# Kernel tuning notes

Measured on AMD Instinct MI355X. Metric: run time of the kernel, lower is better.

The kernel has to match this reference:

```python
import jax, jax.numpy as jnp
import numpy as np
import math

B, C, H, W = 32, 384, 64, 64      # batch, backbone dim, feature-map HxW
E, NH = 256, 16                   # embed_dim, num_heads (grapsules per image)
HD = E // NH                      # head dim
RFF_HALF, HID = 32, 128           # RFF rows (out=64), GNN hidden


def setup_inputs() -> dict:
    key = jax.random.key(0)
    ks = jax.random.split(key, 10)
    rn = lambda k, s: (0.02 * jax.random.normal(k, s)).astype(jnp.float32)
    x = jax.random.normal(ks[0], (B, C, H, W), jnp.float32)
    qw = rn(ks[1], (E, C)); qb = jnp.zeros((E,), jnp.float32)
    kw = rn(ks[2], (E, C)); kb = jnp.zeros((E,), jnp.float32)
    vw = rn(ks[3], (E, C)); vb = jnp.zeros((E,), jnp.float32)
    # RFF B ~ N(0,1) * sigma * 2*pi, sigma=1.0
    B_rff = (jax.random.normal(ks[4], (RFF_HALF, 2)) * (2.0 * math.pi)).astype(jnp.float32)
    msg_w = rn(ks[5], (HID, E)); msg_b = jnp.zeros((HID,), jnp.float32)
    emb_w = rn(ks[6], (HID, 2 * RFF_HALF))
    lin1_w = rn(ks[7], (4 * HID, HID)); lin1_b = jnp.zeros((4 * HID,), jnp.float32)
    lin2_w = rn(ks[8], (E, 4 * HID)); lin2_b = jnp.zeros((E,), jnp.float32)
    layer_scale = jnp.full((1, E), 1e-6, jnp.float32)
    # fully-connected directed graph (no self loops) among the NH grapsules of each image
    pairs = np.array([(i, j) for i in range(NH) for j in range(NH) if i != j], dtype=np.int32)
    off = (np.arange(B, dtype=np.int32) * NH)[:, None]
    edge_src = jnp.asarray((pairs[:, 0][None, :] + off).reshape(-1))
    edge_dst = jnp.asarray((pairs[:, 1][None, :] + off).reshape(-1))
    return dict(x=x, qw=qw, qb=qb, kw=kw, kb=kb, vw=vw, vb=vb, B_rff=B_rff,
                msg_w=msg_w, msg_b=msg_b, emb_w=emb_w, lin1_w=lin1_w, lin1_b=lin1_b,
                lin2_w=lin2_w, lin2_b=lin2_b, layer_scale=layer_scale,
                edge_src=edge_src, edge_dst=edge_dst)


def _forward(x, qw, qb, kw, kb, vw, vb, B_rff, msg_w, msg_b, emb_w,
             lin1_w, lin1_b, lin2_w, lin2_b, layer_scale, edge_src, edge_dst):
    Bsz, Cc, Hh, Ww = x.shape
    N = Hh * Ww
    # --- ImageToGraphTransformer (attention pooling to grapsule nodes) ---
    xf = x.reshape(Bsz, Cc, N).transpose(0, 2, 1)            # [B,N,C]
    xm = xf.mean(axis=1)                                     # [B,C]
    q = (xm @ qw.T + qb).reshape(Bsz, NH, HD)                # [B,h,d]
    k = (xf @ kw.T + kb).reshape(Bsz, N, NH, HD)             # [B,N,h,d]
    v = xf @ vw.T + vb                                       # [B,N,E]
    logits = jnp.einsum('bhc,bnhc->bnh', q, k) / math.sqrt(HD)
    attn = jax.nn.softmax(logits, axis=1)                    # softmax over pixels
    xx, yy = jnp.meshgrid(jnp.arange(Hh, dtype=x.dtype), jnp.arange(Ww, dtype=x.dtype), indexing='ij')
    pos_grid = jnp.stack((xx.reshape(-1), yy.reshape(-1)), axis=-1)  # [N,2]
    values = jnp.einsum('bnh,bnc->bhc', attn, v).reshape(Bsz * NH, E)
    pos = jnp.einsum('bnh,nx->bhx', attn, pos_grid).reshape(Bsz * NH, 2)
    # --- RFF embedding of relative positions (edge_attr) ---
    rel = pos[edge_src] - pos[edge_dst]                      # [Eg,2]
    proj = rel @ B_rff.T                                     # [Eg,32]
    edge_attr = math.sqrt(2.0) * jnp.concatenate((jnp.sin(proj), jnp.cos(proj)), axis=-1)
    # --- Conv (MessagePassing) with ConditionalLinear 'strong', mean aggr ---
    m = (values[edge_src] @ msg_w.T + msg_b) * (edge_attr @ emb_w.T)   # [Eg,HID]
    agg = jax.ops.segment_sum(m, edge_dst, num_segments=Bsz * NH) / (NH - 1)
    # --- ConvBlockNeXt MLP + layer scale + identity skip (in==out) ---
    h = jax.nn.silu(agg @ lin1_w.T + lin1_b)
    o = h @ lin2_w.T + lin2_b
    return layer_scale * o + values


def reference(x, qw, qb, kw, kb, vw, vb, B_rff, msg_w, msg_b, emb_w,
              lin1_w, lin1_b, lin2_w, lin2_b, layer_scale, edge_src, edge_dst):
    return _forward(x, qw, qb, kw, kb, vw, vb, B_rff, msg_w, msg_b, emb_w,
                    lin1_w, lin1_b, lin2_w, lin2_b, layer_scale, edge_src, edge_dst)
```

## Files before the change

### kernel.cpp

```cpp
#include <hip/hip_runtime.h>
#include <math.h>


#define Bsz 32
#define Cc  384
#define Nn  4096
#define Ee  256
#define NHh 16
#define HIDh 128

__device__ __forceinline__ float waveSum(float v){
#pragma unroll
  for(int o=32;o;o>>=1) v += __shfl_down(v,(unsigned)o,64);
  return v;
}
__device__ __forceinline__ float waveMaxAll(float v){
#pragma unroll
  for(int o=1;o<64;o<<=1) v = fmaxf(v, __shfl_xor(v,(unsigned)o,64));
  return v;
}
__device__ __forceinline__ float waveSumAll(float v){
#pragma unroll
  for(int o=1;o<64;o<<=1) v += __shfl_xor(v,(unsigned)o,64);
  return v;
}
__device__ __forceinline__ float blockSum(float v, float* sm){
  int lane = threadIdx.x & 63, w = threadIdx.x >> 6;
  int nw = blockDim.x >> 6;
  float r = waveSum(v);
  if(lane==0) sm[w] = r;
  __syncthreads();
  float s = 0.f;
  for(int i=0;i<nw;i++) s += sm[i];
  __syncthreads();
  return s;
}

__global__ __launch_bounds__(256) void k_mean(const float* __restrict__ x, float* __restrict__ xm){
  int bc = blockIdx.x, t = threadIdx.x;
  const float4* xr = (const float4*)(x + (size_t)bc*Nn);
  float s = 0.f;
#pragma unroll
  for(int i=0;i<4;i++){ float4 v = xr[t + 256*i]; s += (v.x+v.y) + (v.z+v.w); }
  __shared__ float sm[8];
  s = blockSum(s, sm);
  if(t==0) xm[bc] = s * (1.0f/4096.0f);
}

__global__ __launch_bounds__(384) void k_qk(const float* __restrict__ xm, const float* __restrict__ qw,
                                            const float* __restrict__ qb, const float* __restrict__ kw,
                                            float* __restrict__ qk_t){
  int b = blockIdx.x, t = threadIdx.x;
  __shared__ float xs[Cc];
  __shared__ float qs[Ee];
  if(t < 96) ((float4*)xs)[t] = ((const float4*)(xm + b*Cc))[t];
  __syncthreads();
  if(t < Ee){
    const float4* wr = (const float4*)(qw + (size_t)t*Cc);
    const float4* xv = (const float4*)xs;
    float a = qb[t];
#pragma unroll 4
    for(int c4=0;c4<96;c4++){ float4 w = wr[c4], xx = xv[c4]; a += w.x*xx.x + w.y*xx.y + w.z*xx.z + w.w*xx.w; }
    qs[t] = a;
  }
  __syncthreads();
  int c = t;
#pragma unroll
  for(int hq=0; hq<4; hq++){
    float r0, r1, r2, r3;
#pragma unroll
    for(int hh=0; hh<4; hh++){
      int h = hq*4 + hh;
      float a = 0.f;
#pragma unroll
      for(int d=0; d<16; d++) a += qs[h*16+d] * kw[(size_t)(h*16+d)*Cc + c];
      a *= 0.25f;
      if(hh==0) r0=a; else if(hh==1) r1=a; else if(hh==2) r2=a; else r3=a;
    }
    ((float4*)(qk_t + ((size_t)b*Cc + c)*16))[hq] = make_float4(r0,r1,r2,r3);
  }
}

__global__ __launch_bounds__(256) void k_logits(const float* __restrict__ x, const float* __restrict__ qk_t,
                                                float* __restrict__ lg, float* __restrict__ spart){
  __shared__ float qks[Cc*16];
  int b = blockIdx.y, ns = blockIdx.x, t = threadIdx.x;
  int n = ns*256 + t;
  {
    const float4* src = (const float4*)(qk_t + (size_t)b*Cc*16);
    float4* dst = (float4*)qks;
#pragma unroll
    for(int i=0;i<6;i++) dst[t + 256*i] = src[t + 256*i];
  }
  __syncthreads();
  float acc[16];
#pragma unroll
  for(int h=0;h<16;h++) acc[h] = 0.f;
  const float* xb = x + (size_t)b*Cc*Nn + n;
#pragma unroll 8
  for(int c=0;c<Cc;c++){
    float xv = xb[(size_t)c*Nn];
    const float4* qv = (const float4*)(qks + c*16);
    float4 q0 = qv[0], q1 = qv[1], q2 = qv[2], q3 = qv[3];
    acc[0]  += xv*q0.x; acc[1]  += xv*q0.y; acc[2]  += xv*q0.z; acc[3]  += xv*q0.w;
    acc[4]  += xv*q1.x; acc[5]  += xv*q1.y; acc[6]  += xv*q1.z; acc[7]  += xv*q1.w;
    acc[8]  += xv*q2.x; acc[9]  += xv*q2.y; acc[10] += xv*q2.z; acc[11] += xv*q2.w;
    acc[12] += xv*q3.x; acc[13] += xv*q3.y; acc[14] += xv*q3.z; acc[15] += xv*q3.w;
  }
#pragma unroll
  for(int h=0;h<16;h++) lg[((size_t)(b*16+h))*Nn + n] = acc[h];

  __syncthreads();
  float* sl = qks;
#pragma unroll
  for(int h=0;h<16;h++) sl[h*256 + t] = acc[h];
  __syncthreads();
  int w = t >> 6, lane = t & 63;
#pragma unroll
  for(int hh=0; hh<4; hh++){
    int h = w*4 + hh;
    float v0 = sl[h*256 + lane], v1 = sl[h*256 + 64 + lane];
    float v2 = sl[h*256 + 128 + lane], v3 = sl[h*256 + 192 + lane];
    float m = waveMaxAll(fmaxf(fmaxf(v0,v1), fmaxf(v2,v3)));
    float e0 = __expf(v0-m), e1 = __expf(v1-m), e2 = __expf(v2-m), e3 = __expf(v3-m);
    float row0 = (float)(ns*4);
    float col  = (float)lane;
    float s  = (e0+e1)+(e2+e3);
    float px = e0*row0 + e1*(row0+1.f) + e2*(row0+2.f) + e3*(row0+3.f);
    float py = s * col;
    float s_t  = waveSumAll(s);
    float px_t = waveSumAll(px);
    float py_t = waveSumAll(py);
    if(lane==0)
      *(float4*)(spart + ((size_t)(b*16+h)*16 + ns)*4) = make_float4(m, s_t, px_t, py_t);
  }
}

#define XROW 36
__global__ __launch_bounds__(256) void k_xa(const float* __restrict__ x, const float* __restrict__ lg,
                                            const float* __restrict__ spart, float* __restrict__ pos,
                                            float* __restrict__ part){
  __shared__ float xl[Cc*XROW];
  __shared__ float al[NHh*XROW];
  __shared__ float ss[32];
  int b = blockIdx.y, ns = blockIdx.x, t = threadIdx.x;
  int th = t & 3, tc = t >> 2;
  if(t < 64){
    int h = t >> 2, qq = t & 3;
    const float4* sp = (const float4*)spart + (size_t)(b*16+h)*16 + qq*4;
    float4 p0 = sp[0], p1 = sp[1], p2 = sp[2], p3 = sp[3];
    float m = fmaxf(fmaxf(p0.x,p1.x), fmaxf(p2.x,p3.x));
    m = fmaxf(m, __shfl_xor(m, 1u, 64));
    m = fmaxf(m, __shfl_xor(m, 2u, 64));
    float w0 = __expf(p0.x-m), w1 = __expf(p1.x-m), w2 = __expf(p2.x-m), w3 = __expf(p3.x-m);
    float s  = p0.y*w0 + p1.y*w1 + p2.y*w2 + p3.y*w3;
    float px = p0.z*w0 + p1.z*w1 + p2.z*w2 + p3.z*w3;
    float py = p0.w*w0 + p1.w*w1 + p2.w*w2 + p3.w*w3;
    s  += __shfl_xor(s, 1u, 64);  s  += __shfl_xor(s, 2u, 64);
    px += __shfl_xor(px,1u, 64);  px += __shfl_xor(px,2u, 64);
    py += __shfl_xor(py,1u, 64);  py += __shfl_xor(py,2u, 64);
    if(qq==0){
      float inv = 1.0f/s;
      ss[h*2] = m; ss[h*2+1] = inv;
      if(ns==0){ pos[(b*16+h)*2] = px*inv; pos[(b*16+h)*2+1] = py*inv; }
    }
  }
  __syncthreads();
  int ah = t >> 3, aj = t & 7;
  float mA = 0.f, iA = 0.f;
  if(t < 128){ mA = ss[ah*2]; iA = ss[ah*2+1]; }
  float acc[4][6];
#pragma unroll
  for(int k=0;k<4;k++)
#pragma unroll
    for(int m=0;m<6;m++) acc[k][m] = 0.f;

  float4 xr[12];
  float4 ar = make_float4(0,0,0,0);

  auto LOAD = [&](int ch){
    int n0 = ns*256 + ch*32;
    if(t < 128)
      ar = *(const float4*)(lg + ((size_t)(b*16+ah))*Nn + n0 + aj*4);
#pragma unroll
    for(int i=0;i<12;i++){
      int f = t + 256*i;
      int c = f >> 3, j4 = f & 7;
      xr[i] = *(const float4*)(x + ((size_t)(b*Cc+c))*Nn + n0 + j4*4);
    }
  };

  LOAD(0);
  for(int ch=0; ch<8; ch++){
    if(t < 128){
      float4 e;
      e.x = __expf(ar.x - mA)*iA;
      e.y = __expf(ar.y - mA)*iA;
      e.z = __expf(ar.z - mA)*iA;
      e.w = __expf(ar.w - mA)*iA;
      *(float4*)(al + ah*XROW + aj*4) = e;
    }
#pragma unroll
    for(int i=0;i<12;i++){
      int f = t + 256*i;
      int c = f >> 3, j4 = f & 7;
      *(float4*)(xl + c*XROW + j4*4) = xr[i];
    }
    __syncthreads();
    if(ch < 7) LOAD(ch+1);
#pragma unroll
    for(int j4=0;j4<8;j4++){
      float4 a4[4], x4[6];
#pragma unroll
      for(int k=0;k<4;k++) a4[k] = *(const float4*)(al + (th+4*k)*XROW + j4*4);
#pragma unroll
      for(int m=0;m<6;m++) x4[m] = *(const float4*)(xl + (tc+64*m)*XROW + j4*4);
#pragma unroll
      for(int k=0;k<4;k++)
#pragma unroll
        for(int m=0;m<6;m++)
          acc[k][m] += a4[k].x*x4[m].x + a4[k].y*x4[m].y + a4[k].z*x4[m].z + a4[k].w*x4[m].w;
    }
    __syncthreads();
  }
#pragma unroll
  for(int k=0;k<4;k++)
#pragma unroll
    for(int m=0;m<6;m++)
      part[(size_t)ns*(Bsz*NHh*Cc) + (size_t)(b*16 + th + 4*k)*Cc + (tc + 64*m)] = acc[k][m];
}

__global__ __launch_bounds__(256) void k_values(const float* __restrict__ part, const float* __restrict__ vw,
                                                const float* __restrict__ vb, const float* __restrict__ msg_w,
                                                const float* __restrict__ msg_b,
                                                float* __restrict__ values, float* __restrict__ msgv){
  int node = blockIdx.x, t = threadIdx.x;
  __shared__ float xa[Cc];
  __shared__ float vs[Ee];
  if(t < 96){
    float4 s = make_float4(0,0,0,0);
#pragma unroll
    for(int p=0;p<16;p++){
      float4 v = *(const float4*)(part + (size_t)p*(Bsz*NHh*Cc) + (size_t)node*Cc + t*4);
      s.x += v.x; s.y += v.y; s.z += v.z; s.w += v.w;
    }
    *(float4*)(xa + t*4) = s;
  }
  __syncthreads();
  {
    const float4* wr = (const float4*)(vw + (size_t)t*Cc);
    const float4* xv = (const float4*)xa;
    float a = vb[t];
#pragma unroll 4
    for(int c4=0;c4<96;c4++){ float4 w = wr[c4], xx = xv[c4]; a += w.x*xx.x + w.y*xx.y + w.z*xx.z + w.w*xx.w; }
    values[(size_t)node*Ee + t] = a;
    vs[t] = a;
  }
  __syncthreads();
  if(t < HIDh){
    const float4* mr = (const float4*)(msg_w + (size_t)t*Ee);
    const float4* vv = (const float4*)vs;
    float a = msg_b[t];
#pragma unroll 4
    for(int e4=0;e4<64;e4++){ float4 w = mr[e4], xx = vv[e4]; a += w.x*xx.x + w.y*xx.y + w.z*xx.z + w.w*xx.w; }
    msgv[(size_t)node*HIDh + t] = a;
  }
}

__global__ __launch_bounds__(128) void k_agg(const float* __restrict__ pos, const float* __restrict__ msgv,
                                             const float* __restrict__ brff, const float* __restrict__ emb_w,
                                             float* __restrict__ agg){
  int node = blockIdx.x, t = threadIdx.x;
  int b = node >> 4, jj = node & 15;
  __shared__ float ps[32];
  __shared__ float bf[64];
  __shared__ float mv[16*HIDh];
  __shared__ float ea[64];
  if(t < 32) ps[t] = pos[b*32 + t];
  if(t < 64) bf[t] = brff[t];
#pragma unroll
  for(int i=0;i<4;i++){ int f = t + 128*i; ((float4*)mv)[f] = ((const float4*)(msgv + (size_t)b*16*HIDh))[f]; }
  float4 er[16];
#pragma unroll
  for(int i=0;i<16;i++) er[i] = ((const float4*)(emb_w + (size_t)t*64))[i];
  __syncthreads();
  float pxj = ps[jj*2], pyj = ps[jj*2+1];
  float acc = 0.f;
  for(int i=0;i<16;i++){
    if(i == jj) continue;
    float rx = ps[i*2]   - pxj;
    float ry = ps[i*2+1] - pyj;
    __syncthreads();
    if(t < 32){
      float pr = rx*bf[t*2] + ry*bf[t*2+1];
      ea[t]    = 1.41421356f * __sinf(pr);
      ea[t+32] = 1.41421356f * __cosf(pr);
    }
    __syncthreads();
    float psi = 0.f;
    const float4* eav = (const float4*)ea;
#pragma unroll
    for(int k=0;k<16;k++){ float4 e4 = eav[k]; psi += e4.x*er[k].x + e4.y*er[k].y + e4.z*er[k].z + e4.w*er[k].w; }
    acc += mv[i*HIDh + t] * psi;
  }
  agg[(size_t)node*HIDh + t] = acc * (1.0f/15.0f);
}

__global__ __launch_bounds__(256) void k_mlp(const float* __restrict__ agg, const float* __restrict__ l1w,
                                             const float* __restrict__ l1b, const float* __restrict__ l2w,
                                             const float* __restrict__ l2b, const float* __restrict__ ls,
                                             const float* __restrict__ values, float* __restrict__ out){
  int node = blockIdx.x, t = threadIdx.x;
  __shared__ float ag[HIDh];
  __shared__ float h1[512];
  if(t < 32) ((float4*)ag)[t] = ((const float4*)(agg + (size_t)node*HIDh))[t];
  __syncthreads();
#pragma unroll
  for(int r=0;r<2;r++){
    int u = t + r*256;
    const float4* wr = (const float4*)(l1w + (size_t)u*HIDh);
    const float4* av = (const float4*)ag;
    float a = l1b[u];
#pragma unroll 4
    for(int k=0;k<32;k++){ float4 w = wr[k], xx = av[k]; a += w.x*xx.x + w.y*xx.y + w.z*xx.z + w.w*xx.w; }
    h1[u] = a / (1.0f + __expf(-a));
  }
  __syncthreads();
  {
    const float4* wr = (const float4*)(l2w + (size_t)t*512);
    const float4* hv = (const float4*)h1;
    float o = l2b[t];
#pragma unroll 4
    for(int k=0;k<128;k++){ float4 w = wr[k], xx = hv[k]; o += w.x*xx.x + w.y*xx.y + w.z*xx.z + w.w*xx.w; }
    size_t oi = (size_t)node*Ee + t;
    out[oi] = ls[t]*o + values[oi];
  }
}

extern "C" void kernel_launch(void* const* d_in, const int* in_sizes, int n_in,
                              void* d_out, int out_size, void* d_ws, size_t ws_size,
                              hipStream_t stream) {
  const float* x    = (const float*)d_in[0];
  const float* qw   = (const float*)d_in[1];
  const float* qb   = (const float*)d_in[2];
  const float* kw   = (const float*)d_in[3];
  const float* vw   = (const float*)d_in[5];
  const float* vb   = (const float*)d_in[6];
  const float* brff = (const float*)d_in[7];
  const float* msgw = (const float*)d_in[8];
  const float* msgb = (const float*)d_in[9];
  const float* embw = (const float*)d_in[10];
  const float* l1w  = (const float*)d_in[11];
  const float* l1b  = (const float*)d_in[12];
  const float* l2w  = (const float*)d_in[13];
  const float* l2b  = (const float*)d_in[14];
  const float* lsc  = (const float*)d_in[15];

  float* W      = (float*)d_ws;
  float* xm     = W;
  float* qkt    = xm  + 12288;
  float* lg     = qkt + 196608;
  float* pos    = lg  + 2097152;
  float* spart  = pos + 1024;
  float* part   = spart + 32768;
  float* values = part + 3145728;
  float* msgv   = values + 131072;
  float* agg    = msgv + 65536;
  float* out    = (float*)d_out;

  k_mean  <<<Bsz*Cc, 256, 0, stream>>>(x, xm);
  k_qk    <<<Bsz, 384, 0, stream>>>(xm, qw, qb, kw, qkt);
  k_logits<<<dim3(16, Bsz), 256, 0, stream>>>(x, qkt, lg, spart);
  k_xa    <<<dim3(16, Bsz), 256, 0, stream>>>(x, lg, spart, pos, part);
  k_values<<<Bsz*NHh, 256, 0, stream>>>(part, vw, vb, msgw, msgb, values, msgv);
  k_agg   <<<Bsz*NHh, 128, 0, stream>>>(pos, msgv, brff, embw, agg);
  k_mlp   <<<Bsz*NHh, 256, 0, stream>>>(agg, l1w, l1b, l2w, l2b, lsc, values, out);
}
```

Measured before the change: 564.9 us.

## Split k_xa over channel halves and read qk directly from global in k_logits

k_xa now splits the 384 channels into two halves across blocks, so the grid doubles to 1024 blocks. Each block uses half the shared memory and accumulators, which is meant to raise occupancy and parallelism on a grid that was previously only 512 blocks. Partial sums go into 32 slots, and k_values is changed to reduce the two halves from separate slot ranges. Separately, k_logits stops staging qk in LDS and reads it straight from global/cache, dropping a sync and 24KB of shared memory. The cost is that the logits and softmax coefficients are recomputed per half-block, and the x reads in k_logits now compete with uniform global loads of qk.

New measurement: 579.5 us. +2.6%, slower.

```diff
diff --git a/kernel.cpp b/kernel.cpp
--- a/kernel.cpp
+++ b/kernel.cpp
@@ -83,25 +83,18 @@
 
 __global__ __launch_bounds__(256) void k_logits(const float* __restrict__ x, const float* __restrict__ qk_t,
                                                 float* __restrict__ lg, float* __restrict__ spart){
-  __shared__ float qks[Cc*16];
+  __shared__ float sl[16*256];
   int b = blockIdx.y, ns = blockIdx.x, t = threadIdx.x;
   int n = ns*256 + t;
-  {
-    const float4* src = (const float4*)(qk_t + (size_t)b*Cc*16);
-    float4* dst = (float4*)qks;
-#pragma unroll
-    for(int i=0;i<6;i++) dst[t + 256*i] = src[t + 256*i];
-  }
-  __syncthreads();
   float acc[16];
 #pragma unroll
   for(int h=0;h<16;h++) acc[h] = 0.f;
   const float* xb = x + (size_t)b*Cc*Nn + n;
+  const float4* qk = (const float4*)(qk_t + (size_t)b*Cc*16);
 #pragma unroll 8
   for(int c=0;c<Cc;c++){
     float xv = xb[(size_t)c*Nn];
-    const float4* qv = (const float4*)(qks + c*16);
-    float4 q0 = qv[0], q1 = qv[1], q2 = qv[2], q3 = qv[3];
+    float4 q0 = qk[c*4+0], q1 = qk[c*4+1], q2 = qk[c*4+2], q3 = qk[c*4+3];
     acc[0]  += xv*q0.x; acc[1]  += xv*q0.y; acc[2]  += xv*q0.z; acc[3]  += xv*q0.w;
     acc[4]  += xv*q1.x; acc[5]  += xv*q1.y; acc[6]  += xv*q1.z; acc[7]  += xv*q1.w;
     acc[8]  += xv*q2.x; acc[9]  += xv*q2.y; acc[10] += xv*q2.z; acc[11] += xv*q2.w;
@@ -110,8 +103,6 @@
 #pragma unroll
   for(int h=0;h<16;h++) lg[((size_t)(b*16+h))*Nn + n] = acc[h];
 
-  __syncthreads();
-  float* sl = qks;
 #pragma unroll
   for(int h=0;h<16;h++) sl[h*256 + t] = acc[h];
   __syncthreads();
@@ -137,13 +128,16 @@
 }
 
 #define XROW 36
+#define CSPL 192
+#define SLOTSZ (512*CSPL)
 __global__ __launch_bounds__(256) void k_xa(const float* __restrict__ x, const float* __restrict__ lg,
                                             const float* __restrict__ spart, float* __restrict__ pos,
                                             float* __restrict__ part){
-  __shared__ float xl[Cc*XROW];
+  __shared__ float xl[CSPL*XROW];
   __shared__ float al[NHh*XROW];
   __shared__ float ss[32];
-  int b = blockIdx.y, ns = blockIdx.x, t = threadIdx.x;
+  int b = blockIdx.y, t = threadIdx.x;
+  int ns = blockIdx.x & 15, cs = blockIdx.x >> 4;
   int th = t & 3, tc = t >> 2;
   if(t < 64){
     int h = t >> 2, qq = t & 3;
@@ -162,31 +156,32 @@
     if(qq==0){
       float inv = 1.0f/s;
       ss[h*2] = m; ss[h*2+1] = inv;
-      if(ns==0){ pos[(b*16+h)*2] = px*inv; pos[(b*16+h)*2+1] = py*inv; }
+      if(blockIdx.x==0){ pos[(b*16+h)*2] = px*inv; pos[(b*16+h)*2+1] = py*inv; }
     }
   }
   __syncthreads();
   int ah = t >> 3, aj = t & 7;
   float mA = 0.f, iA = 0.f;
   if(t < 128){ mA = ss[ah*2]; iA = ss[ah*2+1]; }
-  float acc[4][6];
+  float acc[4][3];
 #pragma unroll
   for(int k=0;k<4;k++)
 #pragma unroll
-    for(int m=0;m<6;m++) acc[k][m] = 0.f;
-
-  float4 xr[12];
+    for(int m=0;m<3;m++) acc[k][m] = 0.f;
+
+  float4 xr[6];
   float4 ar = make_float4(0,0,0,0);
+  const float* xbase = x + ((size_t)b*Cc + (size_t)cs*CSPL)*Nn;
 
   auto LOAD = [&](int ch){
     int n0 = ns*256 + ch*32;
     if(t < 128)
       ar = *(const float4*)(lg + ((size_t)(b*16+ah))*Nn + n0 + aj*4);
 #pragma unroll
-    for(int i=0;i<12;i++){
+    for(int i=0;i<6;i++){
       int f = t + 256*i;
       int c = f >> 3, j4 = f & 7;
-      xr[i] = *(const float4*)(x + ((size_t)(b*Cc+c))*Nn + n0 + j4*4);
+      xr[i] = *(const float4*)(xbase + (size_t)c*Nn + n0 + j4*4);
     }
   };
 
@@ -201,7 +196,7 @@
       *(float4*)(al + ah*XROW + aj*4) = e;
     }
 #pragma unroll
-    for(int i=0;i<12;i++){
+    for(int i=0;i<6;i++){
       int f = t + 256*i;
       int c = f >> 3, j4 = f & 7;
       *(float4*)(xl + c*XROW + j4*4) = xr[i];
@@ -210,24 +205,25 @@
     if(ch < 7) LOAD(ch+1);
 #pragma unroll
     for(int j4=0;j4<8;j4++){
-      float4 a4[4], x4[6];
+      float4 a4[4], x4[3];
 #pragma unroll
       for(int k=0;k<4;k++) a4[k] = *(const float4*)(al + (th+4*k)*XROW + j4*4);
 #pragma unroll
-      for(int m=0;m<6;m++) x4[m] = *(const float4*)(xl + (tc+64*m)*XROW + j4*4);
+      for(int m=0;m<3;m++) x4[m] = *(const float4*)(xl + (tc+64*m)*XROW + j4*4);
 #pragma unroll
       for(int k=0;k<4;k++)
 #pragma unroll
-        for(int m=0;m<6;m++)
+        for(int m=0;m<3;m++)
           acc[k][m] += a4[k].x*x4[m].x + a4[k].y*x4[m].y + a4[k].z*x4[m].z + a4[k].w*x4[m].w;
     }
     __syncthreads();
   }
+  size_t slot = (size_t)(cs*16 + ns)*SLOTSZ;
 #pragma unroll
   for(int k=0;k<4;k++)
 #pragma unroll
-    for(int m=0;m<6;m++)
-      part[(size_t)ns*(Bsz*NHh*Cc) + (size_t)(b*16 + th + 4*k)*Cc + (tc + 64*m)] = acc[k][m];
+    for(int m=0;m<3;m++)
+      part[slot + (size_t)(b*16 + th + 4*k)*CSPL + (tc + 64*m)] = acc[k][m];
 }
 
 __global__ __launch_bounds__(256) void k_values(const float* __restrict__ part, const float* __restrict__ vw,
@@ -238,10 +234,12 @@
   __shared__ float xa[Cc];
   __shared__ float vs[Ee];
   if(t < 96){
+    int half = (t >= 48);
+    const float* base = part + (size_t)(half*16)*SLOTSZ + (size_t)node*CSPL + (t*4 - half*CSPL);
     float4 s = make_float4(0,0,0,0);
 #pragma unroll
     for(int p=0;p<16;p++){
-      float4 v = *(const float4*)(part + (size_t)p*(Bsz*NHh*Cc) + (size_t)node*Cc + t*4);
+      float4 v = *(const float4*)(base + (size_t)p*SLOTSZ);
       s.x += v.x; s.y += v.y; s.z += v.z; s.w += v.w;
     }
     *(float4*)(xa + t*4) = s;
@@ -371,7 +369,7 @@
   k_mean  <<<Bsz*Cc, 256, 0, stream>>>(x, xm);
   k_qk    <<<Bsz, 384, 0, stream>>>(xm, qw, qb, kw, qkt);
   k_logits<<<dim3(16, Bsz), 256, 0, stream>>>(x, qkt, lg, spart);
-  k_xa    <<<dim3(16, Bsz), 256, 0, stream>>>(x, lg, spart, pos, part);
+  k_xa    <<<dim3(32, Bsz), 256, 0, stream>>>(x, lg, spart, pos, part);
   k_values<<<Bsz*NHh, 256, 0, stream>>>(part, vw, vb, msgw, msgb, values, msgv);
   k_agg   <<<Bsz*NHh, 128, 0, stream>>>(pos, msgv, brff, embw, agg);
   k_mlp   <<<Bsz*NHh, 256, 0, stream>>>(agg, l1w, l1b, l2w, l2b, lsc, values, out);
```

## Fuse logits and attention pooling with flash-style partial softmax rescaling

Applied to the files above, without the earlier changes.

Merges the logits kernel and the attention-weighted pooling kernel into one. Each block keeps its unnormalized exponentials in shared memory, writes unnormalized partial pooled sums, and the values kernel rescales the partials using the per-tile max and sum statistics. This removes the global logits buffer round trip and a second pass reading the logits. The aggregation and MLP kernels are also merged, and the qk table is now read directly from global memory instead of staged in LDS. The cost is higher LDS use per block, which can lower occupancy.

Result: slower. 585.8 us (+3.7%).

```diff
diff --git a/kernel.cpp b/kernel.cpp
--- a/kernel.cpp
+++ b/kernel.cpp
@@ -81,107 +81,70 @@
   }
 }
 
-__global__ __launch_bounds__(256) void k_logits(const float* __restrict__ x, const float* __restrict__ qk_t,
-                                                float* __restrict__ lg, float* __restrict__ spart){
-  __shared__ float qks[Cc*16];
+#define XROW 36
+#define ELS  260
+__global__ __launch_bounds__(256) void k_attn(const float* __restrict__ x, const float* __restrict__ qk_t,
+                                              float* __restrict__ spart, float* __restrict__ part){
+  __shared__ float el[16*ELS];
+  __shared__ float xl[Cc*XROW];
   int b = blockIdx.y, ns = blockIdx.x, t = threadIdx.x;
   int n = ns*256 + t;
+
+  float acc[16];
+#pragma unroll
+  for(int h=0;h<16;h++) acc[h] = 0.f;
   {
-    const float4* src = (const float4*)(qk_t + (size_t)b*Cc*16);
-    float4* dst = (float4*)qks;
-#pragma unroll
-    for(int i=0;i<6;i++) dst[t + 256*i] = src[t + 256*i];
-  }
-  __syncthreads();
-  float acc[16];
-#pragma unroll
-  for(int h=0;h<16;h++) acc[h] = 0.f;
-  const float* xb = x + (size_t)b*Cc*Nn + n;
-#pragma unroll 8
-  for(int c=0;c<Cc;c++){
-    float xv = xb[(size_t)c*Nn];
-    const float4* qv = (const float4*)(qks + c*16);
-    float4 q0 = qv[0], q1 = qv[1], q2 = qv[2], q3 = qv[3];
-    acc[0]  += xv*q0.x; acc[1]  += xv*q0.y; acc[2]  += xv*q0.z; acc[3]  += xv*q0.w;
-    acc[4]  += xv*q1.x; acc[5]  += xv*q1.y; acc[6]  += xv*q1.z; acc[7]  += xv*q1.w;
-    acc[8]  += xv*q2.x; acc[9]  += xv*q2.y; acc[10] += xv*q2.z; acc[11] += xv*q2.w;
-    acc[12] += xv*q3.x; acc[13] += xv*q3.y; acc[14] += xv*q3.z; acc[15] += xv*q3.w;
-  }
-#pragma unroll
-  for(int h=0;h<16;h++) lg[((size_t)(b*16+h))*Nn + n] = acc[h];
-
-  __syncthreads();
-  float* sl = qks;
-#pragma unroll
-  for(int h=0;h<16;h++) sl[h*256 + t] = acc[h];
-  __syncthreads();
-  int w = t >> 6, lane = t & 63;
-#pragma unroll
-  for(int hh=0; hh<4; hh++){
-    int h = w*4 + hh;
-    float v0 = sl[h*256 + lane], v1 = sl[h*256 + 64 + lane];
-    float v2 = sl[h*256 + 128 + lane], v3 = sl[h*256 + 192 + lane];
-    float m = waveMaxAll(fmaxf(fmaxf(v0,v1), fmaxf(v2,v3)));
-    float e0 = __expf(v0-m), e1 = __expf(v1-m), e2 = __expf(v2-m), e3 = __expf(v3-m);
-    float row0 = (float)(ns*4);
-    float col  = (float)lane;
-    float s  = (e0+e1)+(e2+e3);
-    float px = e0*row0 + e1*(row0+1.f) + e2*(row0+2.f) + e3*(row0+3.f);
-    float py = s * col;
-    float s_t  = waveSumAll(s);
-    float px_t = waveSumAll(px);
-    float py_t = waveSumAll(py);
-    if(lane==0)
-      *(float4*)(spart + ((size_t)(b*16+h)*16 + ns)*4) = make_float4(m, s_t, px_t, py_t);
-  }
-}
-
-#define XROW 36
-__global__ __launch_bounds__(256) void k_xa(const float* __restrict__ x, const float* __restrict__ lg,
-                                            const float* __restrict__ spart, float* __restrict__ pos,
-                                            float* __restrict__ part){
-  __shared__ float xl[Cc*XROW];
-  __shared__ float al[NHh*XROW];
-  __shared__ float ss[32];
-  int b = blockIdx.y, ns = blockIdx.x, t = threadIdx.x;
+    const float* xb = x + (size_t)b*Cc*Nn + n;
+    const float4* qk = (const float4*)(qk_t + (size_t)b*Cc*16);
+#pragma unroll 16
+    for(int c=0;c<Cc;c++){
+      float xv = xb[(size_t)c*Nn];
+      float4 q0 = qk[c*4+0], q1 = qk[c*4+1], q2 = qk[c*4+2], q3 = qk[c*4+3];
+      acc[0]  += xv*q0.x; acc[1]  += xv*q0.y; acc[2]  += xv*q0.z; acc[3]  += xv*q0.w;
+      acc[4]  += xv*q1.x; acc[5]  += xv*q1.y; acc[6]  += xv*q1.z; acc[7]  += xv*q1.w;
+      acc[8]  += xv*q2.x; acc[9]  += xv*q2.y; acc[10] += xv*q2.z; acc[11] += xv*q2.w;
+      acc[12] += xv*q3.x; acc[13] += xv*q3.y; acc[14] += xv*q3.z; acc[15] += xv*q3.w;
+    }
+  }
+
+#pragma unroll
+  for(int h=0;h<16;h++) el[h*ELS + t] = acc[h];
+  __syncthreads();
+  {
+    int w = t >> 6, lane = t & 63;
+#pragma unroll
+    for(int hh=0; hh<4; hh++){
+      int h = w*4 + hh;
+      float v0 = el[h*ELS + lane],       v1 = el[h*ELS + 64 + lane];
+      float v2 = el[h*ELS + 128 + lane], v3 = el[h*ELS + 192 + lane];
+      float m = waveMaxAll(fmaxf(fmaxf(v0,v1), fmaxf(v2,v3)));
+      float e0 = __expf(v0-m), e1 = __expf(v1-m), e2 = __expf(v2-m), e3 = __expf(v3-m);
+      el[h*ELS + lane]       = e0;  el[h*ELS + 64 + lane]  = e1;
+      el[h*ELS + 128 + lane] = e2;  el[h*ELS + 192 + lane] = e3;
+      float row0 = (float)(ns*4);
+      float col  = (float)lane;
+      float s  = (e0+e1)+(e2+e3);
+      float px = e0*row0 + e1*(row0+1.f) + e2*(row0+2.f) + e3*(row0+3.f);
+      float py = s * col;
+      float s_t  = waveSumAll(s);
+      float px_t = waveSumAll(px);
+      float py_t = waveSumAll(py);
+      if(lane==0)
+        *(float4*)(spart + ((size_t)(b*16+h)*16 + ns)*4) = make_float4(m, s_t, px_t, py_t);
+    }
+  }
+  __syncthreads();
+
   int th = t & 3, tc = t >> 2;
-  if(t < 64){
-    int h = t >> 2, qq = t & 3;
-    const float4* sp = (const float4*)spart + (size_t)(b*16+h)*16 + qq*4;
-    float4 p0 = sp[0], p1 = sp[1], p2 = sp[2], p3 = sp[3];
-    float m = fmaxf(fmaxf(p0.x,p1.x), fmaxf(p2.x,p3.x));
-    m = fmaxf(m, __shfl_xor(m, 1u, 64));
-    m = fmaxf(m, __shfl_xor(m, 2u, 64));
-    float w0 = __expf(p0.x-m), w1 = __expf(p1.x-m), w2 = __expf(p2.x-m), w3 = __expf(p3.x-m);
-    float s  = p0.y*w0 + p1.y*w1 + p2.y*w2 + p3.y*w3;
-    float px = p0.z*w0 + p1.z*w1 + p2.z*w2 + p3.z*w3;
-    float py = p0.w*w0 + p1.w*w1 + p2.w*w2 + p3.w*w3;
-    s  += __shfl_xor(s, 1u, 64);  s  += __shfl_xor(s, 2u, 64);
-    px += __shfl_xor(px,1u, 64);  px += __shfl_xor(px,2u, 64);
-    py += __shfl_xor(py,1u, 64);  py += __shfl_xor(py,2u, 64);
-    if(qq==0){
-      float inv = 1.0f/s;
-      ss[h*2] = m; ss[h*2+1] = inv;
-      if(ns==0){ pos[(b*16+h)*2] = px*inv; pos[(b*16+h)*2+1] = py*inv; }
-    }
-  }
-  __syncthreads();
-  int ah = t >> 3, aj = t & 7;
-  float mA = 0.f, iA = 0.f;
-  if(t < 128){ mA = ss[ah*2]; iA = ss[ah*2+1]; }
-  float acc[4][6];
+  float acc2[4][6];
 #pragma unroll
   for(int k=0;k<4;k++)
 #pragma unroll
-    for(int m=0;m<6;m++) acc[k][m] = 0.f;
+    for(int m=0;m<6;m++) acc2[k][m] = 0.f;
 
   float4 xr[12];
-  float4 ar = make_float4(0,0,0,0);
-
   auto LOAD = [&](int ch){
     int n0 = ns*256 + ch*32;
-    if(t < 128)
-      ar = *(const float4*)(lg + ((size_t)(b*16+ah))*Nn + n0 + aj*4);
 #pragma unroll
     for(int i=0;i<12;i++){
       int f = t + 256*i;
@@ -192,14 +155,6 @@
 
   LOAD(0);
   for(int ch=0; ch<8; ch++){
-    if(t < 128){
-      float4 e;
-      e.x = __expf(ar.x - mA)*iA;
-      e.y = __expf(ar.y - mA)*iA;
-      e.z = __expf(ar.z - mA)*iA;
-      e.w = __expf(ar.w - mA)*iA;
-      *(float4*)(al + ah*XROW + aj*4) = e;
-    }
 #pragma unroll
     for(int i=0;i<12;i++){
       int f = t + 256*i;
@@ -208,18 +163,19 @@
     }
     __syncthreads();
     if(ch < 7) LOAD(ch+1);
+    int n0l = ch*32;
 #pragma unroll
     for(int j4=0;j4<8;j4++){
       float4 a4[4], x4[6];
 #pragma unroll
-      for(int k=0;k<4;k++) a4[k] = *(const float4*)(al + (th+4*k)*XROW + j4*4);
+      for(int k=0;k<4;k++) a4[k] = *(const float4*)(el + (th+4*k)*ELS + n0l + j4*4);
 #pragma unroll
       for(int m=0;m<6;m++) x4[m] = *(const float4*)(xl + (tc+64*m)*XROW + j4*4);
 #pragma unroll
       for(int k=0;k<4;k++)
 #pragma unroll
         for(int m=0;m<6;m++)
-          acc[k][m] += a4[k].x*x4[m].x + a4[k].y*x4[m].y + a4[k].z*x4[m].z + a4[k].w*x4[m].w;
+          acc2[k][m] += a4[k].x*x4[m].x + a4[k].y*x4[m].y + a4[k].z*x4[m].z + a4[k].w*x4[m].w;
     }
     __syncthreads();
   }
@@ -227,24 +183,50 @@
   for(int k=0;k<4;k++)
 #pragma unroll
     for(int m=0;m<6;m++)
-      part[(size_t)ns*(Bsz*NHh*Cc) + (size_t)(b*16 + th + 4*k)*Cc + (tc + 64*m)] = acc[k][m];
-}
-
-__global__ __launch_bounds__(256) void k_values(const float* __restrict__ part, const float* __restrict__ vw,
-                                                const float* __restrict__ vb, const float* __restrict__ msg_w,
-                                                const float* __restrict__ msg_b,
-                                                float* __restrict__ values, float* __restrict__ msgv){
+      part[(size_t)ns*(Bsz*NHh*Cc) + (size_t)(b*16 + th + 4*k)*Cc + (tc + 64*m)] = acc2[k][m];
+}
+
+__global__ __launch_bounds__(256) void k_values(const float* __restrict__ part, const float* __restrict__ spart,
+                                                const float* __restrict__ vw, const float* __restrict__ vb,
+                                                const float* __restrict__ msg_w, const float* __restrict__ msg_b,
+                                                float* __restrict__ values, float* __restrict__ msgv,
+                                                float* __restrict__ pos){
   int node = blockIdx.x, t = threadIdx.x;
   __shared__ float xa[Cc];
   __shared__ float vs[Ee];
+  __shared__ float scl[16];
+  __shared__ float invs;
+  if(t < 16){
+    float4 sp = ((const float4*)spart)[node*16 + t];
+    float M = sp.x;
+    M = fmaxf(M, __shfl_xor(M,1u,64)); M = fmaxf(M, __shfl_xor(M,2u,64));
+    M = fmaxf(M, __shfl_xor(M,4u,64)); M = fmaxf(M, __shfl_xor(M,8u,64));
+    float wgt = __expf(sp.x - M);
+    float s = sp.y*wgt, px = sp.z*wgt, py = sp.w*wgt;
+    s  += __shfl_xor(s,1u,64);  s  += __shfl_xor(s,2u,64);
+    s  += __shfl_xor(s,4u,64);  s  += __shfl_xor(s,8u,64);
+    px += __shfl_xor(px,1u,64); px += __shfl_xor(px,2u,64);
+    px += __shfl_xor(px,4u,64); px += __shfl_xor(px,8u,64);
+    py += __shfl_xor(py,1u,64); py += __shfl_xor(py,2u,64);
+    py += __shfl_xor(py,4u,64); py += __shfl_xor(py,8u,64);
+    scl[t] = wgt;
+    if(t==0){
+      float iv = 1.0f/s;
+      invs = iv;
+      pos[node*2] = px*iv; pos[node*2+1] = py*iv;
+    }
+  }
+  __syncthreads();
   if(t < 96){
+    float iv = invs;
     float4 s = make_float4(0,0,0,0);
 #pragma unroll
     for(int p=0;p<16;p++){
       float4 v = *(const float4*)(part + (size_t)p*(Bsz*NHh*Cc) + (size_t)node*Cc + t*4);
-      s.x += v.x; s.y += v.y; s.z += v.z; s.w += v.w;
-    }
-    *(float4*)(xa + t*4) = s;
+      float sc = scl[p];
+      s.x += v.x*sc; s.y += v.y*sc; s.z += v.z*sc; s.w += v.w*sc;
+    }
+    *(float4*)(xa + t*4) = make_float4(s.x*iv, s.y*iv, s.z*iv, s.w*iv);
   }
   __syncthreads();
   {
@@ -267,22 +249,28 @@
   }
 }
 
-__global__ __launch_bounds__(128) void k_agg(const float* __restrict__ pos, const float* __restrict__ msgv,
-                                             const float* __restrict__ brff, const float* __restrict__ emb_w,
-                                             float* __restrict__ agg){
+__global__ __launch_bounds__(256) void k_aggmlp(const float* __restrict__ pos, const float* __restrict__ msgv,
+        const float* __restrict__ brff, const float* __restrict__ emb_w,
+        const float* __restrict__ l1w, const float* __restrict__ l1b,
+        const float* __restrict__ l2w, const float* __restrict__ l2b,
+        const float* __restrict__ ls, const float* __restrict__ values, float* __restrict__ out){
   int node = blockIdx.x, t = threadIdx.x;
   int b = node >> 4, jj = node & 15;
   __shared__ float ps[32];
   __shared__ float bf[64];
   __shared__ float mv[16*HIDh];
   __shared__ float ea[64];
+  __shared__ float ag[HIDh];
+  __shared__ float h1[512];
   if(t < 32) ps[t] = pos[b*32 + t];
   if(t < 64) bf[t] = brff[t];
 #pragma unroll
-  for(int i=0;i<4;i++){ int f = t + 128*i; ((float4*)mv)[f] = ((const float4*)(msgv + (size_t)b*16*HIDh))[f]; }
+  for(int i=0;i<2;i++){ int f = t + 256*i; ((float4*)mv)[f] = ((const float4*)(msgv + (size_t)b*16*HIDh))[f]; }
   float4 er[16];
-#pragma unroll
-  for(int i=0;i<16;i++) er[i] = ((const float4*)(emb_w + (size_t)t*64))[i];
+  if(t < HIDh){
+#pragma unroll
+    for(int k=0;k<16;k++) er[k] = ((const float4*)(emb_w + (size_t)t*64))[k];
+  }
   __syncthreads();
   float pxj = ps[jj*2], pyj = ps[jj*2+1];
   float acc = 0.f;
@@ -297,23 +285,15 @@
       ea[t+32] = 1.41421356f * __cosf(pr);
     }
     __syncthreads();
-    float psi = 0.f;
-    const float4* eav = (const float4*)ea;
-#pragma unroll
-    for(int k=0;k<16;k++){ float4 e4 = eav[k]; psi += e4.x*er[k].x + e4.y*er[k].y + e4.z*er[k].z + e4.w*er[k].w; }
-    acc += mv[i*HIDh + t] * psi;
-  }
-  agg[(size_t)node*HIDh + t] = acc * (1.0f/15.0f);
-}
-
-__global__ __launch_bounds__(256) void k_mlp(const float* __restrict__ agg, const float* __restrict__ l1w,
-                                             const float* __restrict__ l1b, const float* __restrict__ l2w,
-                                             const float* __restrict__ l2b, const float* __restrict__ ls,
-                                             const float* __restrict__ values, float* __restrict__ out){
-  int node = blockIdx.x, t = threadIdx.x;
-  __shared__ float ag[HIDh];
-  __shared__ float h1[512];
-  if(t < 32) ((float4*)ag)[t] = ((const float4*)(agg + (size_t)node*HIDh))[t];
+    if(t < HIDh){
+      float psi = 0.f;
+      const float4* eav = (const float4*)ea;
+#pragma unroll
+      for(int k=0;k<16;k++){ float4 e4 = eav[k]; psi += e4.x*er[k].x + e4.y*er[k].y + e4.z*er[k].z + e4.w*er[k].w; }
+      acc += mv[i*HIDh + t] * psi;
+    }
+  }
+  if(t < HIDh) ag[t] = acc * (1.0f/15.0f);
   __syncthreads();
 #pragma unroll
   for(int r=0;r<2;r++){
@@ -359,20 +339,16 @@
   float* W      = (float*)d_ws;
   float* xm     = W;
   float* qkt    = xm  + 12288;
-  float* lg     = qkt + 196608;
-  float* pos    = lg  + 2097152;
-  float* spart  = pos + 1024;
+  float* spart  = qkt + 196608;
   float* part   = spart + 32768;
   float* values = part + 3145728;
   float* msgv   = values + 131072;
-  float* agg    = msgv + 65536;
+  float* pos    = msgv + 65536;
   float* out    = (float*)d_out;
 
   k_mean  <<<Bsz*Cc, 256, 0, stream>>>(x, xm);
   k_qk    <<<Bsz, 384, 0, stream>>>(xm, qw, qb, kw, qkt);
-  k_logits<<<dim3(16, Bsz), 256, 0, stream>>>(x, qkt, lg, spart);
-  k_xa    <<<dim3(16, Bsz), 256, 0, stream>>>(x, lg, spart, pos, part);
-  k_values<<<Bsz*NHh, 256, 0, stream>>>(part, vw, vb, msgw, msgb, values, msgv);
-  k_agg   <<<Bsz*NHh, 128, 0, stream>>>(pos, msgv, brff, embw, agg);
-  k_mlp   <<<Bsz*NHh, 256, 0, stream>>>(agg, l1w, l1b, l2w, l2b, lsc, values, out);
-}
+  k_attn  <<<dim3(16, Bsz), 256, 0, stream>>>(x, qkt, spart, part);
+  k_values<<<Bsz*NHh, 256, 0, stream>>>(part, spart, vw, vb, msgw, msgb, values, msgv, pos);
+  k_aggmlp<<<Bsz*NHh, 256, 0, stream>>>(pos, msgv, brff, embw, l1w, l1b, l2w, l2b, lsc, values, out);
+}
```
